# Optimization experiments

Measured on AMD Instinct MI355X. Metric: run time of the kernel, lower is better.

The kernel has to match this reference:

```python
import jax, jax.numpy as jnp
import numpy as np

D = 64       # CNF state dimension
H = 512      # MLP hidden width
B = 8192     # batch


def setup_inputs() -> dict:
    key = jax.random.key(0)
    ks = jax.random.split(key, 8)
    s1 = 1.0 / np.sqrt(D + 1)
    s2 = 1.0 / np.sqrt(H)
    return {
        "t": jax.random.uniform(ks[0], (1,), dtype=jnp.float32),
        "x": jax.random.normal(ks[1], (B, D + 1), dtype=jnp.float32),
        "W1": jax.random.normal(ks[2], (D + 1, H), dtype=jnp.float32) * s1,
        "b1": jnp.zeros((H,), dtype=jnp.float32),
        "W2": jax.random.normal(ks[3], (H, H), dtype=jnp.float32) * s2,
        "b2": jnp.zeros((H,), dtype=jnp.float32),
        "W3": jax.random.normal(ks[4], (H, D), dtype=jnp.float32) * s2,
        "b3": jnp.zeros((D,), dtype=jnp.float32),
    }


def reference(t, x, W1, b1, W2, b2, W3, b3):
    # CNF.forward: strip log-density channel, evaluate vf and its exact divergence.
    xs = x[..., :-1]                      # [B, D]
    tt = t[0]

    def vf_single(xi):                    # xi: [D] -> [D]
        inp = jnp.concatenate([tt[None], xi])          # vf(t*ones, x) with t prepended
        h = jnp.tanh(inp @ W1 + b1)
        h = jnp.tanh(h @ W2 + b2)
        return h @ W3 + b3

    dx = jax.vmap(vf_single)(xs)                        # [B, D]
    # exact divergence: trace of per-sample Jacobian via reverse-mode (matches torch jacrev)
    J = jax.vmap(jax.jacrev(vf_single))(xs)             # [B, D, D]
    div = jnp.trace(J, axis1=-2, axis2=-1)              # [B]
    return jnp.concatenate([dx, div[:, None]], axis=-1) # [B, D+1]
```

## Files before the change

### kernel.cpp

```cpp
#include <hip/hip_runtime.h>

#define HH 512
#define DD 64
#define MROWS 32
#define TPB 1024
#define LP 520

typedef unsigned short u16;
typedef short s16x8 __attribute__((ext_vector_type(8)));
typedef float f32x4 __attribute__((ext_vector_type(4)));

#define MFMA16(A,B,C) __builtin_amdgcn_mfma_f32_16x16x32_bf16((A),(B),(C),0,0,0)

#define OFF_EF   0
#define OFF_W2F  (HH*HH)
#define OFF_W1F  (2*HH*HH)
#define OFF_W3F  (2*HH*HH + HH*DD)
#define OFF_Z0B  ((2*HH*HH + 2*HH*DD)*2)

__device__ __forceinline__ u16 f2bf(float f) {
    unsigned u = __builtin_bit_cast(unsigned, f);
    u += 0x7fffu + ((u >> 16) & 1u);
    return (u16)(u >> 16);
}
__device__ __forceinline__ float bf2f(u16 h) {
    return __builtin_bit_cast(float, (unsigned)h << 16);
}
__device__ __forceinline__ float fast_tanh(float x) {
    float e = __expf(2.0f * x);
    return 1.0f - 2.0f * __builtin_amdgcn_rcpf(e + 1.0f);
}

__global__ __launch_bounds__(256) void precompute(
    const float* __restrict__ t,  const float* __restrict__ W1,
    const float* __restrict__ b1, const float* __restrict__ W2,
    const float* __restrict__ W3, u16* __restrict__ ws16, float* __restrict__ z0)
{
    __shared__ float T[16 * 264 > 256 * 20 ? 16 * 264 : 256 * 20];
    u16* Ef  = ws16 + OFF_EF;
    u16* W2f = ws16 + OFF_W2F;
    u16* W1f = ws16 + OFF_W1F;
    u16* W3f = ws16 + OFF_W3F;

    const int bid = blockIdx.x, tid = threadIdx.x;
    const int lane = tid & 63, wv = tid >> 6;
    const int m16 = lane & 15, q = lane >> 4;

    if (bid < 64) {
        const int nt = bid >> 1, bh = bid & 1;
        const int a0 = nt * 16, b0 = bh * 256;
        s16x8 afh[2], afl[2];
#pragma unroll
        for (int h = 0; h < 2; ++h)
#pragma unroll
            for (int j = 0; j < 8; ++j) {
                int i = h * 32 + q * 8 + j;
                float v = W1[(1 + i) * HH + a0 + m16];
                u16 hi = f2bf(v);
                afh[h][j] = (short)hi;
                afl[h][j] = (short)f2bf(v - bf2f(hi));
            }
#pragma unroll
        for (int bt = 0; bt < 4; ++bt) {
            int bl = wv * 64 + bt * 16;
            s16x8 bfh[2], bfl[2];
#pragma unroll
            for (int h = 0; h < 2; ++h) {
                const float* src = W3 + (b0 + bl + m16) * DD + h * 32 + q * 8;
                float4 p0 = *(const float4*)(src);
                float4 p1 = *(const float4*)(src + 4);
                float vv[8] = {p0.x,p0.y,p0.z,p0.w,p1.x,p1.y,p1.z,p1.w};
#pragma unroll
                for (int j = 0; j < 8; ++j) {
                    u16 hi = f2bf(vv[j]);
                    bfh[h][j] = (short)hi;
                    bfl[h][j] = (short)f2bf(vv[j] - bf2f(hi));
                }
            }
            f32x4 c = {0.f, 0.f, 0.f, 0.f};
#pragma unroll
            for (int h = 0; h < 2; ++h) {
                c = MFMA16(afh[h], bfh[h], c);
                c = MFMA16(afh[h], bfl[h], c);
                c = MFMA16(afl[h], bfh[h], c);
            }
#pragma unroll
            for (int r = 0; r < 4; ++r)
                T[(4 * q + r) * 264 + bl + m16] = c[r];
        }
        __syncthreads();
#pragma unroll
        for (int p = 0; p < 2; ++p) {
            int ksl = p * 4 + wv;
            int al  = m16;
            int blc = ksl * 32 + q * 8;
            const float* w2p = W2 + (a0 + al) * HH + b0 + blc;
            float4 wa = *(const float4*)(w2p), wb = *(const float4*)(w2p + 4);
            const float* glp = T + al * 264 + blc;
            s16x8 o;
            o[0]=(short)f2bf(wa.x*glp[0]); o[1]=(short)f2bf(wa.y*glp[1]);
            o[2]=(short)f2bf(wa.z*glp[2]); o[3]=(short)f2bf(wa.w*glp[3]);
            o[4]=(short)f2bf(wb.x*glp[4]); o[5]=(short)f2bf(wb.y*glp[5]);
            o[6]=(short)f2bf(wb.z*glp[6]); o[7]=(short)f2bf(wb.w*glp[7]);
            *(s16x8*)(Ef + nt * 8192 + (b0 / 32 + ksl) * 512 + lane * 8) = o;
        }
        if (bh == 0 && tid < 128) {
            int ks = tid >> 6, ln = tid & 63;
            int n  = nt * 16 + (ln & 15);
            int k0 = ks * 32 + (ln >> 4) * 8;
            s16x8 o;
#pragma unroll
            for (int j = 0; j < 8; ++j) o[j] = (short)f2bf(W1[(1 + k0 + j) * HH + n]);
            *(s16x8*)(W1f + nt * 1024 + ks * 512 + ln * 8) = o;
        }
    } else if (bid < 128) {
        const int nt = (bid - 64) >> 1, kh = (bid - 64) & 1;
        const int n0 = nt * 16, k0 = kh * 256;
#pragma unroll
        for (int it = 0; it < 4; ++it) {
            int r = (tid >> 2) + it * 64;
            int c = (tid & 3) * 4;
            float4 v = *(const float4*)(W2 + (k0 + r) * HH + n0 + c);
            *(float4*)(T + r * 20 + c) = v;
        }
        __syncthreads();
#pragma unroll
        for (int p = 0; p < 2; ++p) {
            int ksl = p * 4 + wv;
            int kq  = ksl * 32 + q * 8;
            s16x8 o;
#pragma unroll
            for (int j = 0; j < 8; ++j) o[j] = (short)f2bf(T[(kq + j) * 20 + m16]);
            *(s16x8*)(W2f + nt * 8192 + (k0 / 32 + ksl) * 512 + lane * 8) = o;
        }
    } else if (bid < 136) {
        const int ot = (bid - 128) >> 1, kh = (bid - 128) & 1;
        const int o0 = ot * 16, k0 = kh * 256;
#pragma unroll
        for (int it = 0; it < 4; ++it) {
            int r = (tid >> 2) + it * 64;
            int c = (tid & 3) * 4;
            float4 v = *(const float4*)(W3 + (k0 + r) * DD + o0 + c);
            *(float4*)(T + r * 20 + c) = v;
        }
        __syncthreads();
#pragma unroll
        for (int p = 0; p < 2; ++p) {
            int ksl = p * 4 + wv;
            int kq  = ksl * 32 + q * 8;
            s16x8 o;
#pragma unroll
            for (int j = 0; j < 8; ++j) o[j] = (short)f2bf(T[(kq + j) * 20 + m16]);
            *(s16x8*)(W3f + ot * 8192 + (k0 / 32 + ksl) * 512 + lane * 8) = o;
        }
    } else {
        for (int n = tid; n < HH; n += 256)
            z0[n] = b1[n] + t[0] * W1[n];
    }
}

__global__ __launch_bounds__(TPB) void cnf_main(
    const float* __restrict__ x,  const u16* __restrict__ ws16,
    const float* __restrict__ z0, const float* __restrict__ b2,
    const float* __restrict__ b3, float* __restrict__ out)
{
    __shared__ u16 h1s[MROWS * LP];
    __shared__ u16 h2s[MROWS * LP];
    __shared__ u16 d2s[MROWS * LP];
    __shared__ float z0s[HH];
    __shared__ float b2s[HH];
    __shared__ float b3s[DD];
    __shared__ float divacc[16][MROWS];

    const u16* Ef  = ws16 + OFF_EF;
    const u16* W2f = ws16 + OFF_W2F;
    const u16* W1f = ws16 + OFF_W1F;
    const u16* W3f = ws16 + OFF_W3F;

    const int tid  = threadIdx.x;
    const int lane = tid & 63;
    const int w    = tid >> 6;
    const int m16  = lane & 15;
    const int q    = lane >> 4;
    const int kq   = q * 8;
    const int n1   = w * 32;
    const int r0   = blockIdx.x * MROWS;

    u16* xs = d2s;

    s16x8 p1b[2][2];
#pragma unroll
    for (int ct = 0; ct < 2; ++ct) {
        const u16* bb = W1f + (w * 2 + ct) * 1024 + lane * 8;
        p1b[ct][0] = *(const s16x8*)(bb);
        p1b[ct][1] = *(const s16x8*)(bb + 512);
    }
    const u16* w2bp0 = W2f + (2 * w + 0) * 8192 + lane * 8;
    const u16* w2bp1 = W2f + (2 * w + 1) * 8192 + lane * 8;
    s16x8 B0[4], B1[4];
#pragma unroll
    for (int k = 0; k < 4; ++k) {
        B0[k] = *(const s16x8*)(w2bp0 + k * 512);
        B1[k] = *(const s16x8*)(w2bp1 + k * 512);
    }

    for (int idx = tid; idx < MROWS * DD; idx += TPB) {
        int r = idx >> 6, c = idx & 63;
        xs[r * 72 + c] = f2bf(x[(r0 + r) * (DD + 1) + c]);
    }
    if (tid < HH) { z0s[tid] = z0[tid]; b2s[tid] = b2[tid]; }
    if (tid < DD) b3s[tid] = b3[tid];
    __syncthreads();

    float d1reg[2][2][4];

    {
        s16x8 xa[2][2];
#pragma unroll
        for (int rt = 0; rt < 2; ++rt)
#pragma unroll
            for (int h = 0; h < 2; ++h)
                xa[rt][h] = *(const s16x8*)(xs + (rt * 16 + m16) * 72 + h * 32 + kq);
#pragma unroll
        for (int ct = 0; ct < 2; ++ct) {
            int col = n1 + ct * 16 + m16;
#pragma unroll
            for (int rt = 0; rt < 2; ++rt) {
                f32x4 c = {0.f, 0.f, 0.f, 0.f};
                c = MFMA16(xa[rt][0], p1b[ct][0], c);
                c = MFMA16(xa[rt][1], p1b[ct][1], c);
#pragma unroll
                for (int i = 0; i < 4; ++i) {
                    float hv = fast_tanh(c[i] + z0s[col]);
                    h1s[(rt * 16 + 4 * q + i) * LP + col] = f2bf(hv);
                    d1reg[rt][ct][i] = 1.0f - hv * hv;
                }
            }
        }
    }
    __syncthreads();

    f32x4 a00={0,0,0,0}, a01={0,0,0,0}, a10={0,0,0,0}, a11={0,0,0,0};
    {
        const u16* ap0 = h1s + m16 * LP + kq;
        const u16* ap1 = h1s + (16 + m16) * LP + kq;
#pragma unroll
        for (int ks = 0; ks < 16; ++ks) {
            s16x8 f0 = *(const s16x8*)(ap0 + ks * 32);
            s16x8 f1 = *(const s16x8*)(ap1 + ks * 32);
            const int sl = ks & 3;
            a00 = MFMA16(f0, B0[sl], a00);
            a10 = MFMA16(f1, B0[sl], a10);
            a01 = MFMA16(f0, B1[sl], a01);
            a11 = MFMA16(f1, B1[sl], a11);
            if (ks < 12) {
                B0[sl] = *(const s16x8*)(w2bp0 + (ks + 4) * 512);
                B1[sl] = *(const s16x8*)(w2bp1 + (ks + 4) * 512);
            }
        }
    }

    const u16* efp0 = Ef + (2 * w + 0) * 8192 + lane * 8;
    const u16* efp1 = Ef + (2 * w + 1) * 8192 + lane * 8;
    s16x8 E0[4], E1[4];
#pragma unroll
    for (int k = 0; k < 2; ++k) {
        E0[k] = *(const s16x8*)(efp0 + k * 512);
        E1[k] = *(const s16x8*)(efp1 + k * 512);
    }

    {
        f32x4 acc[2][2] = {{a00, a01}, {a10, a11}};
#pragma unroll
        for (int rt = 0; rt < 2; ++rt)
#pragma unroll
            for (int ct = 0; ct < 2; ++ct) {
                int col = n1 + ct * 16 + m16;
#pragma unroll
                for (int i = 0; i < 4; ++i) {
                    int row = rt * 16 + 4 * q + i;
                    float hv = fast_tanh(acc[rt][ct][i] + b2s[col]);
                    h2s[row * LP + col] = f2bf(hv);
                    d2s[row * LP + col] = f2bf(1.0f - hv * hv);
                }
            }
    }
    __syncthreads();

    if (w < 8) {
        const int rowt = w >> 2, ot = w & 3;
        const u16* ap = h2s + (rowt * 16 + m16) * LP + kq;
        const u16* bp = W3f + ot * 8192 + lane * 8;
        s16x8 W3r[4];
#pragma unroll
        for (int k = 0; k < 4; ++k) W3r[k] = *(const s16x8*)(bp + k * 512);
        f32x4 cA = {0.f,0.f,0.f,0.f}, cB = {0.f,0.f,0.f,0.f};
#pragma unroll
        for (int ks = 0; ks < 16; ++ks) {
            s16x8 f = *(const s16x8*)(ap + ks * 32);
            const int sl = ks & 3;
            if (ks & 1) cB = MFMA16(f, W3r[sl], cB);
            else        cA = MFMA16(f, W3r[sl], cA);
            if (ks < 12) W3r[sl] = *(const s16x8*)(bp + (ks + 4) * 512);
        }
        f32x4 c3 = cA + cB;
        int o = ot * 16 + m16;
#pragma unroll
        for (int i = 0; i < 4; ++i)
            out[(r0 + rowt * 16 + 4 * q + i) * (DD + 1) + o] = c3[i] + b3s[o];
    }

    {
        f32x4 g00={0,0,0,0}, g01={0,0,0,0}, g10={0,0,0,0}, g11={0,0,0,0};
        const u16* ap0 = d2s + m16 * LP + kq;
        const u16* ap1 = d2s + (16 + m16) * LP + kq;
#pragma unroll
        for (int ks = 0; ks < 16; ++ks) {
            s16x8 f0 = *(const s16x8*)(ap0 + ks * 32);
            s16x8 f1 = *(const s16x8*)(ap1 + ks * 32);
            const int sl = ks & 3;
            g00 = MFMA16(f0, E0[sl], g00);
            g10 = MFMA16(f1, E0[sl], g10);
            g01 = MFMA16(f0, E1[sl], g01);
            g11 = MFMA16(f1, E1[sl], g11);
            if (ks < 14) {
                const int dl = (ks + 2) & 3;
                E0[dl] = *(const s16x8*)(efp0 + (ks + 2) * 512);
                E1[dl] = *(const s16x8*)(efp1 + (ks + 2) * 512);
            }
        }
        f32x4 acc[2][2] = {{g00, g01}, {g10, g11}};
#pragma unroll
        for (int rt = 0; rt < 2; ++rt)
#pragma unroll
            for (int i = 0; i < 4; ++i) {
                float v = d1reg[rt][0][i] * acc[rt][0][i]
                        + d1reg[rt][1][i] * acc[rt][1][i];
                v += __shfl_xor(v, 1, 64);
                v += __shfl_xor(v, 2, 64);
                v += __shfl_xor(v, 4, 64);
                v += __shfl_xor(v, 8, 64);
                if (m16 == 0) divacc[w][rt * 16 + 4 * q + i] = v;
            }
    }
    __syncthreads();

    if (tid < MROWS) {
        float s = 0.0f;
#pragma unroll
        for (int ww = 0; ww < 16; ++ww) s += divacc[ww][tid];
        out[(r0 + tid) * (DD + 1) + DD] = s;
    }
}

extern "C" void kernel_launch(void* const* d_in, const int* in_sizes, int n_in,
                              void* d_out, int out_size, void* d_ws, size_t ws_size,
                              hipStream_t stream) {
    const float* t  = (const float*)d_in[0];
    const float* x  = (const float*)d_in[1];
    const float* W1 = (const float*)d_in[2];
    const float* b1 = (const float*)d_in[3];
    const float* W2 = (const float*)d_in[4];
    const float* b2 = (const float*)d_in[5];
    const float* W3 = (const float*)d_in[6];
    const float* b3 = (const float*)d_in[7];
    float* out = (float*)d_out;

    u16*   ws16 = (u16*)d_ws;
    float* z0   = (float*)((char*)d_ws + OFF_Z0B);

    precompute<<<137, 256, 0, stream>>>(t, W1, b1, W2, W3, ws16, z0);
    cnf_main<<<8192 / MROWS, TPB, 0, stream>>>(x, ws16, z0, b2, b3, out);
}
```

Baseline: 93.16 us.

## Double rows per block and reuse h2 buffer for derivative tile

Raises the rows per block from 32 to 64 so each wave's register-held W2 and E fragments are reused across four row tiles instead of two. This halves the number of blocks and the per-row cost of loading weights. To fit shared memory, the separate d2 buffer is removed: h2 is overwritten in place with 1-h2^2 after the layer-3 matmul, and d1 is recomputed from the bf16 h1 instead of kept in registers. The risks are more register pressure from the larger accumulator arrays, extra barriers, fewer blocks per GPU, and slightly lower precision for d1 because it now comes from bf16 h1.

```diff
diff --git a/kernel.cpp b/kernel.cpp
--- a/kernel.cpp
+++ b/kernel.cpp
@@ -2,7 +2,7 @@
 
 #define HH 512
 #define DD 64
-#define MROWS 32
+#define MROWS 64
 #define TPB 1024
 #define LP 520
 
@@ -166,7 +166,6 @@
 {
     __shared__ u16 h1s[MROWS * LP];
     __shared__ u16 h2s[MROWS * LP];
-    __shared__ u16 d2s[MROWS * LP];
     __shared__ float z0s[HH];
     __shared__ float b2s[HH];
     __shared__ float b3s[DD];
@@ -186,7 +185,7 @@
     const int n1   = w * 32;
     const int r0   = blockIdx.x * MROWS;
 
-    u16* xs = d2s;
+    u16* xs = h2s;
 
     s16x8 p1b[2][2];
 #pragma unroll
@@ -212,47 +211,58 @@
     if (tid < DD) b3s[tid] = b3[tid];
     __syncthreads();
 
-    float d1reg[2][2][4];
-
     {
-        s16x8 xa[2][2];
-#pragma unroll
-        for (int rt = 0; rt < 2; ++rt)
+        s16x8 xa[4][2];
+#pragma unroll
+        for (int rt = 0; rt < 4; ++rt)
 #pragma unroll
             for (int h = 0; h < 2; ++h)
                 xa[rt][h] = *(const s16x8*)(xs + (rt * 16 + m16) * 72 + h * 32 + kq);
+        float h1v[4][2][4];
 #pragma unroll
         for (int ct = 0; ct < 2; ++ct) {
             int col = n1 + ct * 16 + m16;
 #pragma unroll
-            for (int rt = 0; rt < 2; ++rt) {
+            for (int rt = 0; rt < 4; ++rt) {
                 f32x4 c = {0.f, 0.f, 0.f, 0.f};
                 c = MFMA16(xa[rt][0], p1b[ct][0], c);
                 c = MFMA16(xa[rt][1], p1b[ct][1], c);
 #pragma unroll
-                for (int i = 0; i < 4; ++i) {
-                    float hv = fast_tanh(c[i] + z0s[col]);
-                    h1s[(rt * 16 + 4 * q + i) * LP + col] = f2bf(hv);
-                    d1reg[rt][ct][i] = 1.0f - hv * hv;
-                }
-            }
-        }
-    }
-    __syncthreads();
-
-    f32x4 a00={0,0,0,0}, a01={0,0,0,0}, a10={0,0,0,0}, a11={0,0,0,0};
+                for (int i = 0; i < 4; ++i)
+                    h1v[rt][ct][i] = fast_tanh(c[i] + z0s[col]);
+            }
+        }
+        __syncthreads();
+#pragma unroll
+        for (int ct = 0; ct < 2; ++ct) {
+            int col = n1 + ct * 16 + m16;
+#pragma unroll
+            for (int rt = 0; rt < 4; ++rt)
+#pragma unroll
+                for (int i = 0; i < 4; ++i)
+                    h1s[(rt * 16 + 4 * q + i) * LP + col] = f2bf(h1v[rt][ct][i]);
+        }
+    }
+    __syncthreads();
+
+    f32x4 acc[4][2];
+#pragma unroll
+    for (int rt = 0; rt < 4; ++rt)
+#pragma unroll
+        for (int ct = 0; ct < 2; ++ct) acc[rt][ct] = f32x4{0.f,0.f,0.f,0.f};
     {
-        const u16* ap0 = h1s + m16 * LP + kq;
-        const u16* ap1 = h1s + (16 + m16) * LP + kq;
 #pragma unroll
         for (int ks = 0; ks < 16; ++ks) {
-            s16x8 f0 = *(const s16x8*)(ap0 + ks * 32);
-            s16x8 f1 = *(const s16x8*)(ap1 + ks * 32);
             const int sl = ks & 3;
-            a00 = MFMA16(f0, B0[sl], a00);
-            a10 = MFMA16(f1, B0[sl], a10);
-            a01 = MFMA16(f0, B1[sl], a01);
-            a11 = MFMA16(f1, B1[sl], a11);
+            s16x8 f[4];
+#pragma unroll
+            for (int rt = 0; rt < 4; ++rt)
+                f[rt] = *(const s16x8*)(h1s + (rt * 16 + m16) * LP + ks * 32 + kq);
+#pragma unroll
+            for (int rt = 0; rt < 4; ++rt) {
+                acc[rt][0] = MFMA16(f[rt], B0[sl], acc[rt][0]);
+                acc[rt][1] = MFMA16(f[rt], B1[sl], acc[rt][1]);
+            }
             if (ks < 12) {
                 B0[sl] = *(const s16x8*)(w2bp0 + (ks + 4) * 512);
                 B1[sl] = *(const s16x8*)(w2bp1 + (ks + 4) * 512);
@@ -260,6 +270,41 @@
         }
     }
 
+    const int rowt = w >> 2, ot = w & 3;
+    const u16* w3bp = W3f + ot * 8192 + lane * 8;
+    s16x8 W3r[4];
+#pragma unroll
+    for (int k = 0; k < 4; ++k) W3r[k] = *(const s16x8*)(w3bp + k * 512);
+
+#pragma unroll
+    for (int rt = 0; rt < 4; ++rt)
+#pragma unroll
+        for (int ct = 0; ct < 2; ++ct) {
+            int col = n1 + ct * 16 + m16;
+#pragma unroll
+            for (int i = 0; i < 4; ++i)
+                h2s[(rt * 16 + 4 * q + i) * LP + col] = f2bf(fast_tanh(acc[rt][ct][i] + b2s[col]));
+        }
+    __syncthreads();
+
+    {
+        const u16* ap = h2s + (rowt * 16 + m16) * LP + kq;
+        f32x4 cA = {0.f,0.f,0.f,0.f}, cB = {0.f,0.f,0.f,0.f};
+#pragma unroll
+        for (int ks = 0; ks < 16; ++ks) {
+            s16x8 fA = *(const s16x8*)(ap + ks * 32);
+            const int sl = ks & 3;
+            if (ks & 1) cB = MFMA16(fA, W3r[sl], cB);
+            else        cA = MFMA16(fA, W3r[sl], cA);
+            if (ks < 12) W3r[sl] = *(const s16x8*)(w3bp + (ks + 4) * 512);
+        }
+        f32x4 c3 = cA + cB;
+        int o = ot * 16 + m16;
+#pragma unroll
+        for (int i = 0; i < 4; ++i)
+            out[(r0 + rowt * 16 + 4 * q + i) * (DD + 1) + o] = c3[i] + b3s[o];
+    }
+
     const u16* efp0 = Ef + (2 * w + 0) * 8192 + lane * 8;
     const u16* efp1 = Ef + (2 * w + 1) * 8192 + lane * 8;
     s16x8 E0[4], E1[4];
@@ -268,79 +313,62 @@
         E0[k] = *(const s16x8*)(efp0 + k * 512);
         E1[k] = *(const s16x8*)(efp1 + k * 512);
     }
+    __syncthreads();
+
+#pragma unroll
+    for (int v = 0; v < 4; ++v) {
+        int vi  = tid + v * TPB;
+        int row = vi >> 6, colv = (vi & 63) * 8;
+        u16* p = h2s + row * LP + colv;
+        s16x8 hv = *(const s16x8*)p;
+        s16x8 dv;
+#pragma unroll
+        for (int j = 0; j < 8; ++j) {
+            float f = bf2f((u16)hv[j]);
+            dv[j] = (short)f2bf(1.0f - f * f);
+        }
+        *(s16x8*)p = dv;
+    }
+    __syncthreads();
 
     {
-        f32x4 acc[2][2] = {{a00, a01}, {a10, a11}};
-#pragma unroll
-        for (int rt = 0; rt < 2; ++rt)
-#pragma unroll
-            for (int ct = 0; ct < 2; ++ct) {
-                int col = n1 + ct * 16 + m16;
-#pragma unroll
-                for (int i = 0; i < 4; ++i) {
-                    int row = rt * 16 + 4 * q + i;
-                    float hv = fast_tanh(acc[rt][ct][i] + b2s[col]);
-                    h2s[row * LP + col] = f2bf(hv);
-                    d2s[row * LP + col] = f2bf(1.0f - hv * hv);
-                }
-            }
-    }
-    __syncthreads();
-
-    if (w < 8) {
-        const int rowt = w >> 2, ot = w & 3;
-        const u16* ap = h2s + (rowt * 16 + m16) * LP + kq;
-        const u16* bp = W3f + ot * 8192 + lane * 8;
-        s16x8 W3r[4];
-#pragma unroll
-        for (int k = 0; k < 4; ++k) W3r[k] = *(const s16x8*)(bp + k * 512);
-        f32x4 cA = {0.f,0.f,0.f,0.f}, cB = {0.f,0.f,0.f,0.f};
+        f32x4 g[4][2];
+#pragma unroll
+        for (int rt = 0; rt < 4; ++rt)
+#pragma unroll
+            for (int ct = 0; ct < 2; ++ct) g[rt][ct] = f32x4{0.f,0.f,0.f,0.f};
 #pragma unroll
         for (int ks = 0; ks < 16; ++ks) {
-            s16x8 f = *(const s16x8*)(ap + ks * 32);
             const int sl = ks & 3;
-            if (ks & 1) cB = MFMA16(f, W3r[sl], cB);
-            else        cA = MFMA16(f, W3r[sl], cA);
-            if (ks < 12) W3r[sl] = *(const s16x8*)(bp + (ks + 4) * 512);
-        }
-        f32x4 c3 = cA + cB;
-        int o = ot * 16 + m16;
-#pragma unroll
-        for (int i = 0; i < 4; ++i)
-            out[(r0 + rowt * 16 + 4 * q + i) * (DD + 1) + o] = c3[i] + b3s[o];
-    }
-
-    {
-        f32x4 g00={0,0,0,0}, g01={0,0,0,0}, g10={0,0,0,0}, g11={0,0,0,0};
-        const u16* ap0 = d2s + m16 * LP + kq;
-        const u16* ap1 = d2s + (16 + m16) * LP + kq;
-#pragma unroll
-        for (int ks = 0; ks < 16; ++ks) {
-            s16x8 f0 = *(const s16x8*)(ap0 + ks * 32);
-            s16x8 f1 = *(const s16x8*)(ap1 + ks * 32);
-            const int sl = ks & 3;
-            g00 = MFMA16(f0, E0[sl], g00);
-            g10 = MFMA16(f1, E0[sl], g10);
-            g01 = MFMA16(f0, E1[sl], g01);
-            g11 = MFMA16(f1, E1[sl], g11);
+            s16x8 f[4];
+#pragma unroll
+            for (int rt = 0; rt < 4; ++rt)
+                f[rt] = *(const s16x8*)(h2s + (rt * 16 + m16) * LP + ks * 32 + kq);
+#pragma unroll
+            for (int rt = 0; rt < 4; ++rt) {
+                g[rt][0] = MFMA16(f[rt], E0[sl], g[rt][0]);
+                g[rt][1] = MFMA16(f[rt], E1[sl], g[rt][1]);
+            }
             if (ks < 14) {
                 const int dl = (ks + 2) & 3;
                 E0[dl] = *(const s16x8*)(efp0 + (ks + 2) * 512);
                 E1[dl] = *(const s16x8*)(efp1 + (ks + 2) * 512);
             }
         }
-        f32x4 acc[2][2] = {{g00, g01}, {g10, g11}};
-#pragma unroll
-        for (int rt = 0; rt < 2; ++rt)
+#pragma unroll
+        for (int rt = 0; rt < 4; ++rt)
 #pragma unroll
             for (int i = 0; i < 4; ++i) {
-                float v = d1reg[rt][0][i] * acc[rt][0][i]
-                        + d1reg[rt][1][i] * acc[rt][1][i];
+                int row = rt * 16 + 4 * q + i;
+                float h1a = bf2f(h1s[row * LP + n1 + m16]);
+                float h1b = bf2f(h1s[row * LP + n1 + 16 + m16]);
+                float v = (1.0f - h1a * h1a) * g[rt][0][i]
+                        + (1.0f - h1b * h1b) * g[rt][1][i];
                 v += __shfl_xor(v, 1, 64);
                 v += __shfl_xor(v, 2, 64);
                 v += __shfl_xor(v, 4, 64);
                 v += __shfl_xor(v, 8, 64);
-                if (m16 == 0) divacc[w][rt * 16 + 4 * q + i] = v;
+                if (m16 == 0) divacc[w][row] = v;
             }
     }
     __syncthreads();
```

Measured after the change: 98.25 us. 5.5% more time.

## Stage W2 and Jacobian weights through shared LDS double buffer via async loads

Applied to the files above, without the earlier changes.

The weight tiles for the second layer and the Jacobian-weighted matrix are now laid out k-major. Each k-step chunk is loaded cooperatively by the whole block into a double-buffered LDS area using global_load_lds, instead of every wave streaming its own B fragments from global memory into registers. The separate derivative buffer is removed: the tanh derivative is recomputed in place from the bf16 h2 values after the output GEMM, which frees LDS and registers. The cost is a block-wide barrier on every k-step of both large GEMMs, and a slight loss of precision because the derivative is now computed from rounded h2.

```diff
diff --git a/kernel.cpp b/kernel.cpp
--- a/kernel.cpp
+++ b/kernel.cpp
@@ -12,11 +12,11 @@
 
 #define MFMA16(A,B,C) __builtin_amdgcn_mfma_f32_16x16x32_bf16((A),(B),(C),0,0,0)
 
-#define OFF_EF   0
-#define OFF_W2F  (HH*HH)
-#define OFF_W1F  (2*HH*HH)
-#define OFF_W3F  (2*HH*HH + HH*DD)
-#define OFF_Z0B  ((2*HH*HH + 2*HH*DD)*2)
+#define OFF_W2K  0
+#define OFF_EFK  262144
+#define OFF_W1F  524288
+#define OFF_W3F  557056
+#define OFF_Z0B  (589824 * 2)
 
 __device__ __forceinline__ u16 f2bf(float f) {
     unsigned u = __builtin_bit_cast(unsigned, f);
@@ -29,6 +29,18 @@
 __device__ __forceinline__ float fast_tanh(float x) {
     float e = __expf(2.0f * x);
     return 1.0f - 2.0f * __builtin_amdgcn_rcpf(e + 1.0f);
+}
+
+__device__ __forceinline__ void stage2(const u16* gbase, int chunk, u16* sbuf,
+                                       int w, int lane) {
+#pragma unroll
+    for (int r = 0; r < 2; ++r) {
+        const u16* g = gbase + chunk * 16384 + (2 * w + r) * 512 + lane * 8;
+        u16* l = sbuf + (2 * w + r) * 512;
+        __builtin_amdgcn_global_load_lds(
+            (const __attribute__((address_space(1))) unsigned int*)g,
+            (__attribute__((address_space(3))) unsigned int*)l, 16, 0, 0);
+    }
 }
 
 __global__ __launch_bounds__(256) void precompute(
@@ -37,10 +49,10 @@
     const float* __restrict__ W3, u16* __restrict__ ws16, float* __restrict__ z0)
 {
     __shared__ float T[16 * 264 > 256 * 20 ? 16 * 264 : 256 * 20];
-    u16* Ef  = ws16 + OFF_EF;
-    u16* W2f = ws16 + OFF_W2F;
-    u16* W1f = ws16 + OFF_W1F;
-    u16* W3f = ws16 + OFF_W3F;
+    u16* W2K = ws16 + OFF_W2K;
+    u16* EFK = ws16 + OFF_EFK;
+    u16* W1F = ws16 + OFF_W1F;
+    u16* W3F = ws16 + OFF_W3F;
 
     const int bid = blockIdx.x, tid = threadIdx.x;
     const int lane = tid & 63, wv = tid >> 6;
@@ -102,7 +114,7 @@
             o[2]=(short)f2bf(wa.z*glp[2]); o[3]=(short)f2bf(wa.w*glp[3]);
             o[4]=(short)f2bf(wb.x*glp[4]); o[5]=(short)f2bf(wb.y*glp[5]);
             o[6]=(short)f2bf(wb.z*glp[6]); o[7]=(short)f2bf(wb.w*glp[7]);
-            *(s16x8*)(Ef + nt * 8192 + (b0 / 32 + ksl) * 512 + lane * 8) = o;
+            *(s16x8*)(EFK + (b0 / 32 + ksl) * 16384 + nt * 512 + lane * 8) = o;
         }
         if (bh == 0 && tid < 128) {
             int ks = tid >> 6, ln = tid & 63;
@@ -111,7 +123,7 @@
             s16x8 o;
 #pragma unroll
             for (int j = 0; j < 8; ++j) o[j] = (short)f2bf(W1[(1 + k0 + j) * HH + n]);
-            *(s16x8*)(W1f + nt * 1024 + ks * 512 + ln * 8) = o;
+            *(s16x8*)(W1F + nt * 1024 + ks * 512 + ln * 8) = o;
         }
     } else if (bid < 128) {
         const int nt = (bid - 64) >> 1, kh = (bid - 64) & 1;
@@ -127,11 +139,11 @@
 #pragma unroll
         for (int p = 0; p < 2; ++p) {
             int ksl = p * 4 + wv;
-            int kq  = ksl * 32 + q * 8;
+            int kqx = ksl * 32 + q * 8;
             s16x8 o;
 #pragma unroll
-            for (int j = 0; j < 8; ++j) o[j] = (short)f2bf(T[(kq + j) * 20 + m16]);
-            *(s16x8*)(W2f + nt * 8192 + (k0 / 32 + ksl) * 512 + lane * 8) = o;
+            for (int j = 0; j < 8; ++j) o[j] = (short)f2bf(T[(kqx + j) * 20 + m16]);
+            *(s16x8*)(W2K + (k0 / 32 + ksl) * 16384 + nt * 512 + lane * 8) = o;
         }
     } else if (bid < 136) {
         const int ot = (bid - 128) >> 1, kh = (bid - 128) & 1;
@@ -147,11 +159,11 @@
 #pragma unroll
         for (int p = 0; p < 2; ++p) {
             int ksl = p * 4 + wv;
-            int kq  = ksl * 32 + q * 8;
+            int kqx = ksl * 32 + q * 8;
             s16x8 o;
 #pragma unroll
-            for (int j = 0; j < 8; ++j) o[j] = (short)f2bf(T[(kq + j) * 20 + m16]);
-            *(s16x8*)(W3f + ot * 8192 + (k0 / 32 + ksl) * 512 + lane * 8) = o;
+            for (int j = 0; j < 8; ++j) o[j] = (short)f2bf(T[(kqx + j) * 20 + m16]);
+            *(s16x8*)(W3F + ot * 8192 + (k0 / 32 + ksl) * 512 + lane * 8) = o;
         }
     } else {
         for (int n = tid; n < HH; n += 256)
@@ -166,16 +178,16 @@
 {
     __shared__ u16 h1s[MROWS * LP];
     __shared__ u16 h2s[MROWS * LP];
-    __shared__ u16 d2s[MROWS * LP];
+    __shared__ u16 stg[2][16384];
     __shared__ float z0s[HH];
     __shared__ float b2s[HH];
     __shared__ float b3s[DD];
     __shared__ float divacc[16][MROWS];
 
-    const u16* Ef  = ws16 + OFF_EF;
-    const u16* W2f = ws16 + OFF_W2F;
-    const u16* W1f = ws16 + OFF_W1F;
-    const u16* W3f = ws16 + OFF_W3F;
+    const u16* W2K = ws16 + OFF_W2K;
+    const u16* EFK = ws16 + OFF_EFK;
+    const u16* W1F = ws16 + OFF_W1F;
+    const u16* W3F = ws16 + OFF_W3F;
 
     const int tid  = threadIdx.x;
     const int lane = tid & 63;
@@ -183,26 +195,13 @@
     const int m16  = lane & 15;
     const int q    = lane >> 4;
     const int kq   = q * 8;
-    const int n1   = w * 32;
     const int r0   = blockIdx.x * MROWS;
-
-    u16* xs = d2s;
-
-    s16x8 p1b[2][2];
-#pragma unroll
-    for (int ct = 0; ct < 2; ++ct) {
-        const u16* bb = W1f + (w * 2 + ct) * 1024 + lane * 8;
-        p1b[ct][0] = *(const s16x8*)(bb);
-        p1b[ct][1] = *(const s16x8*)(bb + 512);
-    }
-    const u16* w2bp0 = W2f + (2 * w + 0) * 8192 + lane * 8;
-    const u16* w2bp1 = W2f + (2 * w + 1) * 8192 + lane * 8;
-    s16x8 B0[4], B1[4];
-#pragma unroll
-    for (int k = 0; k < 4; ++k) {
-        B0[k] = *(const s16x8*)(w2bp0 + k * 512);
-        B1[k] = *(const s16x8*)(w2bp1 + k * 512);
-    }
+    const int col0 = 2 * w * 16 + m16;
+    const int col1 = (2 * w + 1) * 16 + m16;
+
+    u16* xs = stg[1];
+
+    stage2(W2K, 0, stg[0], w, lane);
 
     for (int idx = tid; idx < MROWS * DD; idx += TPB) {
         int r = idx >> 6, c = idx & 63;
@@ -210,6 +209,14 @@
     }
     if (tid < HH) { z0s[tid] = z0[tid]; b2s[tid] = b2[tid]; }
     if (tid < DD) b3s[tid] = b3[tid];
+
+    s16x8 p1b[2][2];
+#pragma unroll
+    for (int ct = 0; ct < 2; ++ct) {
+        const u16* bb = W1F + (2 * w + ct) * 1024 + lane * 8;
+        p1b[ct][0] = *(const s16x8*)(bb);
+        p1b[ct][1] = *(const s16x8*)(bb + 512);
+    }
     __syncthreads();
 
     float d1reg[2][2][4];
@@ -223,7 +230,7 @@
                 xa[rt][h] = *(const s16x8*)(xs + (rt * 16 + m16) * 72 + h * 32 + kq);
 #pragma unroll
         for (int ct = 0; ct < 2; ++ct) {
-            int col = n1 + ct * 16 + m16;
+            int col = ct ? col1 : col0;
 #pragma unroll
             for (int rt = 0; rt < 2; ++rt) {
                 f32x4 c = {0.f, 0.f, 0.f, 0.f};
@@ -238,35 +245,21 @@
             }
         }
     }
-    __syncthreads();
 
     f32x4 a00={0,0,0,0}, a01={0,0,0,0}, a10={0,0,0,0}, a11={0,0,0,0};
-    {
-        const u16* ap0 = h1s + m16 * LP + kq;
-        const u16* ap1 = h1s + (16 + m16) * LP + kq;
-#pragma unroll
-        for (int ks = 0; ks < 16; ++ks) {
-            s16x8 f0 = *(const s16x8*)(ap0 + ks * 32);
-            s16x8 f1 = *(const s16x8*)(ap1 + ks * 32);
-            const int sl = ks & 3;
-            a00 = MFMA16(f0, B0[sl], a00);
-            a10 = MFMA16(f1, B0[sl], a10);
-            a01 = MFMA16(f0, B1[sl], a01);
-            a11 = MFMA16(f1, B1[sl], a11);
-            if (ks < 12) {
-                B0[sl] = *(const s16x8*)(w2bp0 + (ks + 4) * 512);
-                B1[sl] = *(const s16x8*)(w2bp1 + (ks + 4) * 512);
-            }
-        }
-    }
-
-    const u16* efp0 = Ef + (2 * w + 0) * 8192 + lane * 8;
-    const u16* efp1 = Ef + (2 * w + 1) * 8192 + lane * 8;
-    s16x8 E0[4], E1[4];
-#pragma unroll
-    for (int k = 0; k < 2; ++k) {
-        E0[k] = *(const s16x8*)(efp0 + k * 512);
-        E1[k] = *(const s16x8*)(efp1 + k * 512);
+#pragma unroll
+    for (int ks = 0; ks < 16; ++ks) {
+        __syncthreads();
+        if (ks < 15) stage2(W2K, ks + 1, stg[(ks + 1) & 1], w, lane);
+        const u16* sb = stg[ks & 1];
+        s16x8 b0 = *(const s16x8*)(sb + (2 * w) * 512 + lane * 8);
+        s16x8 b1v = *(const s16x8*)(sb + (2 * w + 1) * 512 + lane * 8);
+        s16x8 f0 = *(const s16x8*)(h1s + m16 * LP + ks * 32 + kq);
+        s16x8 f1 = *(const s16x8*)(h1s + (16 + m16) * LP + ks * 32 + kq);
+        a00 = MFMA16(f0, b0, a00);
+        a10 = MFMA16(f1, b0, a10);
+        a01 = MFMA16(f0, b1v, a01);
+        a11 = MFMA16(f1, b1v, a11);
     }
 
     {
@@ -275,22 +268,21 @@
         for (int rt = 0; rt < 2; ++rt)
 #pragma unroll
             for (int ct = 0; ct < 2; ++ct) {
-                int col = n1 + ct * 16 + m16;
-#pragma unroll
-                for (int i = 0; i < 4; ++i) {
-                    int row = rt * 16 + 4 * q + i;
-                    float hv = fast_tanh(acc[rt][ct][i] + b2s[col]);
-                    h2s[row * LP + col] = f2bf(hv);
-                    d2s[row * LP + col] = f2bf(1.0f - hv * hv);
-                }
+                int col = ct ? col1 : col0;
+#pragma unroll
+                for (int i = 0; i < 4; ++i)
+                    h2s[(rt * 16 + 4 * q + i) * LP + col] =
+                        f2bf(fast_tanh(acc[rt][ct][i] + b2s[col]));
             }
     }
     __syncthreads();
+
+    stage2(EFK, 0, stg[0], w, lane);
 
     if (w < 8) {
         const int rowt = w >> 2, ot = w & 3;
         const u16* ap = h2s + (rowt * 16 + m16) * LP + kq;
-        const u16* bp = W3f + ot * 8192 + lane * 8;
+        const u16* bp = W3F + ot * 8192 + lane * 8;
         s16x8 W3r[4];
 #pragma unroll
         for (int k = 0; k < 4; ++k) W3r[k] = *(const s16x8*)(bp + k * 512);
@@ -309,25 +301,38 @@
         for (int i = 0; i < 4; ++i)
             out[(r0 + rowt * 16 + 4 * q + i) * (DD + 1) + o] = c3[i] + b3s[o];
     }
+    __syncthreads();
+
+#pragma unroll
+    for (int p = 0; p < 2; ++p) {
+        int g = tid + p * TPB;
+        int row = g >> 6, colv = (g & 63) * 8;
+        u16* pp = h2s + row * LP + colv;
+        s16x8 hv = *(const s16x8*)pp;
+        s16x8 dv;
+#pragma unroll
+        for (int j = 0; j < 8; ++j) {
+            float f = bf2f((u16)hv[j]);
+            dv[j] = (short)f2bf(1.0f - f * f);
+        }
+        *(s16x8*)pp = dv;
+    }
 
     {
         f32x4 g00={0,0,0,0}, g01={0,0,0,0}, g10={0,0,0,0}, g11={0,0,0,0};
-        const u16* ap0 = d2s + m16 * LP + kq;
-        const u16* ap1 = d2s + (16 + m16) * LP + kq;
 #pragma unroll
         for (int ks = 0; ks < 16; ++ks) {
-            s16x8 f0 = *(const s16x8*)(ap0 + ks * 32);
-            s16x8 f1 = *(const s16x8*)(ap1 + ks * 32);
-            const int sl = ks & 3;
-            g00 = MFMA16(f0, E0[sl], g00);
-            g10 = MFMA16(f1, E0[sl], g10);
-            g01 = MFMA16(f0, E1[sl], g01);
-            g11 = MFMA16(f1, E1[sl], g11);
-            if (ks < 14) {
-                const int dl = (ks + 2) & 3;
-                E0[dl] = *(const s16x8*)(efp0 + (ks + 2) * 512);
-                E1[dl] = *(const s16x8*)(efp1 + (ks + 2) * 512);
-            }
+            __syncthreads();
+            if (ks < 15) stage2(EFK, ks + 1, stg[(ks + 1) & 1], w, lane);
+            const u16* sb = stg[ks & 1];
+            s16x8 e0 = *(const s16x8*)(sb + (2 * w) * 512 + lane * 8);
+            s16x8 e1 = *(const s16x8*)(sb + (2 * w + 1) * 512 + lane * 8);
+            s16x8 f0 = *(const s16x8*)(h2s + m16 * LP + ks * 32 + kq);
+            s16x8 f1 = *(const s16x8*)(h2s + (16 + m16) * LP + ks * 32 + kq);
+            g00 = MFMA16(f0, e0, g00);
+            g10 = MFMA16(f1, e0, g10);
+            g01 = MFMA16(f0, e1, g01);
+            g11 = MFMA16(f1, e1, g11);
         }
         f32x4 acc[2][2] = {{g00, g01}, {g10, g11}};
 #pragma unroll
```

Result: slower. 102.3 us (+9.8%).
